# Kernel optimization log

Measured on AMD Instinct MI355X. Metric: run time of the kernel, lower is better.

Reference implementation:

```python
import jax, jax.numpy as jnp
import numpy as np

ALPHA = 1.0
EPS = 1e-8  # torch cosine_similarity default eps


def setup_inputs() -> dict:
    key = jax.random.key(0)
    k1, k2 = jax.random.split(key)
    N, D, J, C = 2048, 64, 20, 3
    predictions = jax.random.normal(k1, (N, D), dtype=jnp.float32)
    data = jax.random.normal(k2, (N, J, C), dtype=jnp.float32)
    return {"predictions": predictions, "data": data}


def reference(predictions, data):
    N = predictions.shape[0]
    # Strict upper triangle i<j. The original loop also includes (i,i) pairs for
    # i < N-1, but those contribute exactly 0 to the loss (dist=0, dis=sqrt(sum(1-1))=0);
    # they only affect the normalizer num = N*(N+1)//2 - 1, which we keep.
    mask = jnp.triu(jnp.ones((N, N), dtype=bool), k=1)

    # Pairwise L2 distances via Gram matrix (avoids [N,N,D] intermediate).
    sq_norms = jnp.sum(predictions * predictions, axis=1)          # [N]
    gram = predictions @ predictions.T                              # [N,N]
    d2 = jnp.maximum(sq_norms[:, None] + sq_norms[None, :] - 2.0 * gram, 0.0)
    dist = jnp.sqrt(jnp.where(mask, d2, 1.0)) * mask                # [N,N], safe sqrt

    # Pairwise bone distance: per-joint cosine similarity over the C axis.
    norms = jnp.sqrt(jnp.sum(data * data, axis=2))                  # [N,J]
    dots = jnp.einsum('ikc,jkc->ijk', data, data)                   # [N,N,J]
    denom = jnp.maximum(norms[:, None, :] * norms[None, :, :], EPS)
    cos = jnp.clip(dots / denom, -1.0, 1.0)
    s = jnp.sum(1.0 - cos * cos, axis=2)                            # [N,N]
    dis = jnp.sqrt(jnp.where(mask, s, 1.0)) * mask                  # safe sqrt

    num = N * (N + 1) // 2 - 1                                      # loop pair count
    loss = jnp.sum(jnp.abs(ALPHA * dist - dis)) / num
    return loss
```

## Files before the change

kernel.cpp:

```cpp
#include <hip/hip_runtime.h>

#define N_PTS 2048
#define D_DIM 64
#define N_J   20
#define LDSW  232
#define T_TILES 32
#define NTILES 528
#define NUM_PAIRS_D 2098175.0

typedef __attribute__((ext_vector_type(8))) short bf16x8;
typedef __attribute__((ext_vector_type(4))) float f32x4;

__device__ inline unsigned short f2bf(float f) {
    union { float f; unsigned int u; } v; v.f = f;
    unsigned int u = v.u;
    return (unsigned short)((u + 0x7FFFu + ((u >> 16) & 1u)) >> 16);
}
__device__ inline unsigned int pack2(float lo, float hi) {
    return (unsigned int)f2bf(lo) | ((unsigned int)f2bf(hi) << 16);
}

__global__ __launch_bounds__(256)
void pairloss_kernel(const float* __restrict__ pred,
                     const float* __restrict__ data,
                     float* __restrict__ partials) {
    __shared__ unsigned short Ash[64 * LDSW];
    __shared__ unsigned short Bsh[64 * LDSW];
    __shared__ float sqA[64], sqB[64], wsum[4];

    int t = blockIdx.x;
    int ib = 0;
    while (t >= T_TILES - ib) { t -= (T_TILES - ib); ++ib; }
    const int jb = ib + t;

    const int tid = threadIdx.x;

    {
        const int half = tid >> 7;
        const int r    = (tid >> 1) & 63;
        const int h    = tid & 1;
        const int grow = (half ? jb : ib) * 64 + r;
        unsigned short* __restrict__ sh = half ? Bsh : Ash;

        const float4* __restrict__ p4 = (const float4*)&pred[grow * D_DIM + h * 32];
        float s = 0.f;
        #pragma unroll
        for (int q = 0; q < 4; ++q) {
            const float4 v0 = p4[2 * q];
            const float4 v1 = p4[2 * q + 1];
            s += v0.x * v0.x + v0.y * v0.y + v0.z * v0.z + v0.w * v0.w;
            s += v1.x * v1.x + v1.y * v1.y + v1.z * v1.z + v1.w * v1.w;
            uint4 u;
            u.x = pack2(v0.x, v0.y);
            u.y = pack2(v0.z, v0.w);
            u.z = pack2(v1.x, v1.y);
            u.w = pack2(v1.z, v1.w);
            *(uint4*)&sh[r * LDSW + h * 32 + q * 8] = u;
        }
        s += __shfl_xor(s, 1);
        if (h == 0) (half ? sqB : sqA)[r] = s;

        const float2* __restrict__ d2 = (const float2*)&data[grow * (N_J * 3) + h * 30];
        float buf[30];
        #pragma unroll
        for (int q = 0; q < 15; ++q) {
            const float2 v = d2[q];
            buf[2 * q] = v.x; buf[2 * q + 1] = v.y;
        }
        const float s2 = 1.4142135623730951f;
        #pragma unroll
        for (int jj = 0; jj < 10; ++jj) {
            float x = buf[3 * jj], y = buf[3 * jj + 1], z = buf[3 * jj + 2];
            const float inv = rsqrtf(fmaxf(x * x + y * y + z * z, 1e-30f));
            x *= inv; y *= inv; z *= inv;
            unsigned int* __restrict__ w32 =
                (unsigned int*)&sh[r * LDSW + D_DIM + (h * 10 + jj) * 6];
            w32[0] = pack2(x * x, y * y);
            w32[1] = pack2(z * z, s2 * x * y);
            w32[2] = pack2(s2 * x * z, s2 * y * z);
        }
        if (h == 1) *(uint4*)&sh[r * LDSW + 184] = (uint4){0u, 0u, 0u, 0u};
    }
    __syncthreads();

    const int w  = tid >> 6;
    const int l  = tid & 63;
    const int lr = l & 15;
    const int kg = l >> 4;

    f32x4 accP[4], accW[4];
    #pragma unroll
    for (int c4 = 0; c4 < 4; ++c4) {
        accP[c4] = (f32x4){0.f, 0.f, 0.f, 0.f};
        accW[c4] = (f32x4){0.f, 0.f, 0.f, 0.f};
    }

    const unsigned short* Abase = &Ash[(w * 16 + lr) * LDSW + kg * 8];
    const unsigned short* Bbase = &Bsh[lr * LDSW + kg * 8];

    #pragma unroll
    for (int ks = 0; ks < 6; ++ks) {
        const bf16x8 af = *(const bf16x8*)(Abase + ks * 32);
        #pragma unroll
        for (int c4 = 0; c4 < 4; ++c4) {
            const bf16x8 bf = *(const bf16x8*)(Bbase + c4 * 16 * LDSW + ks * 32);
            if (ks < 2)
                accP[c4] = __builtin_amdgcn_mfma_f32_16x16x32_bf16(af, bf, accP[c4], 0, 0, 0);
            else
                accW[c4] = __builtin_amdgcn_mfma_f32_16x16x32_bf16(af, bf, accW[c4], 0, 0, 0);
        }
    }

    const int ri0 = w * 16 + kg * 4;
    const int i0  = ib * 64 + ri0;
    float sqi[4];
    #pragma unroll
    for (int r = 0; r < 4; ++r) sqi[r] = sqA[ri0 + r];

    float local = 0.0f;
    #pragma unroll
    for (int c4 = 0; c4 < 4; ++c4) {
        const int jl = c4 * 16 + lr;
        const int j  = jb * 64 + jl;
        const float sqj = sqB[jl];
        #pragma unroll
        for (int r = 0; r < 4; ++r) {
            const int i = i0 + r;
            if (j > i) {
                const float d2   = fmaxf(sqi[r] + sqj - 2.0f * accP[c4][r], 0.0f);
                const float dist = sqrtf(d2);
                const float s    = fmaxf((float)N_J - accW[c4][r], 0.0f);
                local += fabsf(dist - sqrtf(s));
            }
        }
    }

    #pragma unroll
    for (int off = 32; off > 0; off >>= 1) local += __shfl_down(local, off);
    if (l == 0) wsum[w] = local;
    __syncthreads();
    if (tid == 0) partials[blockIdx.x] = wsum[0] + wsum[1] + wsum[2] + wsum[3];
}

__global__ __launch_bounds__(256)
void finalize_kernel(const float* __restrict__ partials, float* __restrict__ out) {
    __shared__ double sh[256];
    double s = 0.0;
    for (int i = threadIdx.x; i < NTILES; i += 256) s += (double)partials[i];
    sh[threadIdx.x] = s;
    __syncthreads();
    for (int off = 128; off > 0; off >>= 1) {
        if (threadIdx.x < off) sh[threadIdx.x] += sh[threadIdx.x + off];
        __syncthreads();
    }
    if (threadIdx.x == 0) out[0] = (float)(sh[0] / NUM_PAIRS_D);
}

extern "C" void kernel_launch(void* const* d_in, const int* in_sizes, int n_in,
                              void* d_out, int out_size, void* d_ws, size_t ws_size,
                              hipStream_t stream) {
    const float* pred = (const float*)d_in[0];
    const float* data = (const float*)d_in[1];
    float* out = (float*)d_out;

    float* partials = (float*)d_ws;

    pairloss_kernel<<<NTILES, 256, 0, stream>>>(pred, data, partials);
    finalize_kernel<<<1, 256, 0, stream>>>(partials, out);
}
```

Before: 19.79 us.

## Tighten LDS layout, closed-form tile index, vectorized stores, wave-shuffle finalize

```diff
diff --git a/kernel.cpp b/kernel.cpp
--- a/kernel.cpp
+++ b/kernel.cpp
@@ -3,7 +3,8 @@
 #define N_PTS 2048
 #define D_DIM 64
 #define N_J   20
-#define LDSW  232
+#define KD    192
+#define LDSW  200
 #define T_TILES 32
 #define NTILES 528
 #define NUM_PAIRS_D 2098175.0
@@ -20,7 +21,7 @@
     return (unsigned int)f2bf(lo) | ((unsigned int)f2bf(hi) << 16);
 }
 
-__global__ __launch_bounds__(256)
+__global__ __launch_bounds__(256, 3)
 void pairloss_kernel(const float* __restrict__ pred,
                      const float* __restrict__ data,
                      float* __restrict__ partials) {
@@ -28,10 +29,14 @@
     __shared__ unsigned short Bsh[64 * LDSW];
     __shared__ float sqA[64], sqB[64], wsum[4];
 
-    int t = blockIdx.x;
-    int ib = 0;
-    while (t >= T_TILES - ib) { t -= (T_TILES - ib); ++ib; }
-    const int jb = ib + t;
+    const int t = blockIdx.x;
+    int ib = (int)((65.0f - sqrtf(4225.0f - 8.0f * (float)t)) * 0.5f);
+    if (ib > T_TILES - 1) ib = T_TILES - 1;
+    if (ib < 0) ib = 0;
+    #define TRI_OFF(i) ((i) * T_TILES - ((i) * ((i) - 1)) / 2)
+    while (ib > 0 && t < TRI_OFF(ib)) --ib;
+    while (ib < T_TILES - 1 && t >= TRI_OFF(ib + 1)) ++ib;
+    const int jb = ib + (t - TRI_OFF(ib));
 
     const int tid = threadIdx.x;
 
@@ -48,8 +53,8 @@
         for (int q = 0; q < 4; ++q) {
             const float4 v0 = p4[2 * q];
             const float4 v1 = p4[2 * q + 1];
-            s += v0.x * v0.x + v0.y * v0.y + v0.z * v0.z + v0.w * v0.w;
-            s += v1.x * v1.x + v1.y * v1.y + v1.z * v1.z + v1.w * v1.w;
+            s += v0.x * v0.x + v0.y * v0.y + v0.z * v0.z + v0.w * v0.w
+               + v1.x * v1.x + v1.y * v1.y + v1.z * v1.z + v1.w * v1.w;
             uint4 u;
             u.x = pack2(v0.x, v0.y);
             u.y = pack2(v0.z, v0.w);
@@ -67,19 +72,25 @@
             const float2 v = d2[q];
             buf[2 * q] = v.x; buf[2 * q + 1] = v.y;
         }
+        unsigned int wreg[32];
         const float s2 = 1.4142135623730951f;
         #pragma unroll
         for (int jj = 0; jj < 10; ++jj) {
             float x = buf[3 * jj], y = buf[3 * jj + 1], z = buf[3 * jj + 2];
             const float inv = rsqrtf(fmaxf(x * x + y * y + z * z, 1e-30f));
             x *= inv; y *= inv; z *= inv;
-            unsigned int* __restrict__ w32 =
-                (unsigned int*)&sh[r * LDSW + D_DIM + (h * 10 + jj) * 6];
-            w32[0] = pack2(x * x, y * y);
-            w32[1] = pack2(z * z, s2 * x * y);
-            w32[2] = pack2(s2 * x * z, s2 * y * z);
+            wreg[3 * jj + 0] = pack2(x * x, y * y);
+            wreg[3 * jj + 1] = pack2(z * z, s2 * x * y);
+            wreg[3 * jj + 2] = pack2(s2 * x * z, s2 * y * z);
         }
-        if (h == 1) *(uint4*)&sh[r * LDSW + 184] = (uint4){0u, 0u, 0u, 0u};
+        wreg[30] = 0u; wreg[31] = 0u;
+        #pragma unroll
+        for (int q = 0; q < 8; ++q) {
+            uint4 u;
+            u.x = wreg[4 * q + 0]; u.y = wreg[4 * q + 1];
+            u.z = wreg[4 * q + 2]; u.w = wreg[4 * q + 3];
+            *(uint4*)&sh[r * LDSW + D_DIM + h * 64 + q * 8] = u;
+        }
     }
     __syncthreads();
 
@@ -98,6 +109,7 @@
     const unsigned short* Abase = &Ash[(w * 16 + lr) * LDSW + kg * 8];
     const unsigned short* Bbase = &Bsh[lr * LDSW + kg * 8];
 
+    __builtin_amdgcn_s_setprio(1);
     #pragma unroll
     for (int ks = 0; ks < 6; ++ks) {
         const bf16x8 af = *(const bf16x8*)(Abase + ks * 32);
@@ -110,6 +122,7 @@
                 accW[c4] = __builtin_amdgcn_mfma_f32_16x16x32_bf16(af, bf, accW[c4], 0, 0, 0);
         }
     }
+    __builtin_amdgcn_s_setprio(0);
 
     const int ri0 = w * 16 + kg * 4;
     const int i0  = ib * 64 + ri0;
@@ -144,16 +157,15 @@
 
 __global__ __launch_bounds__(256)
 void finalize_kernel(const float* __restrict__ partials, float* __restrict__ out) {
-    __shared__ double sh[256];
     double s = 0.0;
     for (int i = threadIdx.x; i < NTILES; i += 256) s += (double)partials[i];
-    sh[threadIdx.x] = s;
+    #pragma unroll
+    for (int off = 32; off > 0; off >>= 1) s += __shfl_down(s, off);
+    __shared__ double sh4[4];
+    if ((threadIdx.x & 63) == 0) sh4[threadIdx.x >> 6] = s;
     __syncthreads();
-    for (int off = 128; off > 0; off >>= 1) {
-        if (threadIdx.x < off) sh[threadIdx.x] += sh[threadIdx.x + off];
-        __syncthreads();
-    }
-    if (threadIdx.x == 0) out[0] = (float)(sh[0] / NUM_PAIRS_D);
+    if (threadIdx.x == 0)
+        out[0] = (float)((sh4[0] + sh4[1] + sh4[2] + sh4[3]) / NUM_PAIRS_D);
 }
 
 extern "C" void kernel_launch(void* const* d_in, const int* in_sizes, int n_in,
```

After: 18.16 us (median of 3 runs). -8.2%, faster.
